# Kernel tuning notes

Measured on AMD Instinct MI355X. Metric: run time of the kernel, lower is better.

## Reference

```python
import jax, jax.numpy as jnp
import numpy as np

EPS = 1e-5


def setup_inputs() -> dict:
    key = jax.random.key(0)
    S, B, I, H, D = 256, 512, 64, 128, 32
    ks = jax.random.split(key, 12)

    def w(k, shape, fan):
        return jax.random.normal(k, shape, jnp.float32) * (fan ** -0.5)

    lengths = jax.random.randint(ks[0], (B,), 1, S + 1)
    lengths = lengths.at[0].set(S)  # ensure max length == S
    return {
        'x': jax.random.normal(ks[1], (S, B, I), jnp.float32),
        'x_d': jax.random.normal(ks[2], (S, B, D), jnp.float32),
        'lengths': lengths,
        'bn_g': jnp.ones((I,), jnp.float32), 'bn_b': jnp.zeros((I,), jnp.float32),
        'bnd_g': jnp.ones((D,), jnp.float32), 'bnd_b': jnp.zeros((D,), jnp.float32),
        'Wih': w(ks[3], (3 * H, I), I), 'Whh': w(ks[4], (3 * H, H), H),
        'bih': jnp.zeros((3 * H,), jnp.float32), 'bhh': jnp.zeros((3 * H,), jnp.float32),
        'attn_W': w(ks[5], (H, H), H), 'attn_b': jnp.zeros((H,), jnp.float32),
        'W1': w(ks[6], (H, H + D), H + D), 'b1': jnp.zeros((H,), jnp.float32),
        'W2': w(ks[7], (H, H), H), 'b2': jnp.zeros((H,), jnp.float32),
        'W3': w(ks[8], (H, H), H), 'b3': jnp.zeros((H,), jnp.float32),
    }


def reference(x, x_d, lengths, bn_g, bn_b, bnd_g, bnd_b, Wih, Whh, bih, bhh,
              attn_W, attn_b, W1, b1, W2, b2, W3, b3):
    S, B, I = x.shape
    H = Whh.shape[1]
    mask = jnp.arange(S)[:, None] < lengths[None, :]          # [S,B] valid-token mask
    mf = mask[..., None].astype(x.dtype)                       # [S,B,1]
    cnt = mf.sum()

    def bn(v, g, b):  # training-mode BatchNorm1d over the packed (valid) tokens
        mu = (v * mf).sum((0, 1)) / cnt
        var = (((v - mu) * mf) ** 2).sum((0, 1)) / cnt
        return (v - mu) * jax.lax.rsqrt(var + EPS) * g + b

    xn = bn(x, bn_g, bn_b)
    xdn = bn(x_d, bnd_g, bnd_b)

    # --- GRU (PyTorch gate order r,z,n) over padded sequence with mask ---
    h0 = jnp.zeros((B, H), x.dtype)

    def step(h, inp):
        xt, mt = inp                                           # xt [B,I], mt [B,1]
        gi = xt @ Wih.T + bih
        gh = h @ Whh.T + bhh
        ir, iz, inn = jnp.split(gi, 3, axis=-1)
        hr, hz, hn = jnp.split(gh, 3, axis=-1)
        r = jax.nn.sigmoid(ir + hr)
        z = jax.nn.sigmoid(iz + hz)
        n = jnp.tanh(inn + r * hn)
        hnew = (1 - z) * n + z * h
        hnext = jnp.where(mt, hnew, h)                         # carry last valid state
        return hnext, jnp.where(mt, hnew, 0.0)                 # padded outputs are 0

    h_last, ys = jax.lax.scan(step, h0, (xn, mf))              # ys [S,B,H]

    # --- Dynamic_Attention: per step i only position j=i survives the causal
    # mask in column k=i, so the dim-0 softmax is over one element -> weight 1.
    # Keep fc in the graph (zero grad, same as torch) via a size-1 softmax. ---
    s = (ys @ attn_W.T + attn_b).sum(-1)                       # [S,B]
    attn = jax.nn.softmax(s[..., None, None], axis=-2)[..., 0, :]  # ones [S,B,1]
    y = attn * ys

    # --- per-token MLP (dropout = identity at eval), vectorized over all tokens ---
    z0 = jnp.concatenate([y, xdn], axis=-1)                    # [S,B,H+D]
    d = jax.nn.relu(z0 @ W1.T + b1)
    d = jax.nn.relu(d @ W2.T + b2)
    d = jax.nn.relu(d @ W3.T + b3)
    out = d * mf                                               # zero padded positions
    return out, h_last[None]                                   # hidden: [1,B,H]
```

## Files before the change

### kernel.cpp

```cpp
#include <hip/hip_runtime.h>
#include <hip/hip_bf16.h>

#define SS 256
#define BB 512
#define II 64
#define HH 128
#define DD 32

typedef __attribute__((ext_vector_type(8))) short short8;
typedef __attribute__((ext_vector_type(4))) float f32x4;

__device__ __forceinline__ short f2bf(float f) {
    unsigned u = __builtin_bit_cast(unsigned, f);
    u += 0x7FFFu + ((u >> 16) & 1u);
    return (short)(u >> 16);
}
__device__ __forceinline__ int pack2bf(float a, float b) {
    return (int)((((unsigned)(unsigned short)f2bf(b)) << 16) |
                  ((unsigned)(unsigned short)f2bf(a)));
}
__device__ __forceinline__ short8 load8bf(const float* p) {
    short8 r;
#pragma unroll
    for (int j = 0; j < 8; ++j) r[j] = f2bf(p[j]);
    return r;
}

__device__ __forceinline__ void sync_lds() {
    __builtin_amdgcn_s_waitcnt(0xc07f);
    __builtin_amdgcn_s_barrier();
}

__global__ __launch_bounds__(256) void stats_kernel(
    const float* __restrict__ x, const float* __restrict__ xd,
    const int* __restrict__ lengths, double* __restrict__ acc)
{
    __shared__ float red_s[256];
    __shared__ float red_q[256];
    const int rows = SS * BB;
    int blk = blockIdx.x;
    const float* v;
    int C, rpb, base;
    if (blk < 256) { v = x;  C = II; rpb = rows / 256; base = 0; }
    else           { v = xd; C = DD; rpb = rows / 128; base = 128; blk -= 256; }

    const int tid = threadIdx.x;
    const int c   = tid & (C - 1);
    const int rg  = tid / C;
    const int rpg = 256 / C;
    const int r0  = blk * rpb;
    const int r1  = r0 + rpb;
    float s = 0.f, q = 0.f;
    for (int r = r0 + rg; r < r1; r += rpg) {
        const int b  = r & (BB - 1);
        const int si = r >> 9;
        if (si < lengths[b]) {
            const float xv = v[(size_t)r * C + c];
            s += xv;
            q  = fmaf(xv, xv, q);
        }
    }
    red_s[tid] = s; red_q[tid] = q;
    __syncthreads();
    if (rg == 0) {
        for (int g = 1; g < rpg; ++g) { s += red_s[c + g * C]; q += red_q[c + g * C]; }
        atomicAdd(&acc[base + c],     (double)s);
        atomicAdd(&acc[base + C + c], (double)q);
    }
}

__global__ __launch_bounds__(128) void finalize_kernel(
    const int* __restrict__ lengths, const double* __restrict__ acc,
    const float* __restrict__ bn_g, const float* __restrict__ bn_b,
    const float* __restrict__ bnd_g, const float* __restrict__ bnd_b,
    float* __restrict__ der)
{
    __shared__ int redc[128];
    __shared__ double s_inv;
    const int tid = threadIdx.x;
    int cs = 0;
    for (int i = tid; i < BB; i += 128) cs += lengths[i];
    redc[tid] = cs;
    __syncthreads();
    if (tid == 0) {
        int tot = 0;
        for (int i = 0; i < 128; ++i) tot += redc[i];
        s_inv = 1.0 / (double)tot;
    }
    __syncthreads();
    const double inv = s_inv;
    if (tid < 64) {
        const double mu  = acc[tid] * inv;
        const double var = acc[64 + tid] * inv - mu * mu;
        const float  rs  = rsqrtf((float)(var + 1e-5));
        const float  a   = rs * bn_g[tid];
        der[tid]      = a;
        der[64 + tid] = bn_b[tid] - (float)mu * a;
    } else if (tid < 96) {
        const int i = tid - 64;
        const double mu  = acc[128 + i] * inv;
        const double var = acc[160 + i] * inv - mu * mu;
        const float  rs  = rsqrtf((float)(var + 1e-5));
        const float  a   = rs * bnd_g[i];
        der[128 + i] = a;
        der[160 + i] = bnd_b[i] - (float)mu * a;
    }
}

__global__ __launch_bounds__(512, 2) void gru_kernel(
    const float* __restrict__ x, const int* __restrict__ lengths,
    const float* __restrict__ Wih, const float* __restrict__ Whh,
    const float* __restrict__ bih, const float* __restrict__ bhh,
    const float* __restrict__ der,
    float* __restrict__ ys, float* __restrict__ hlast)
{
    __shared__ __align__(16) short hbf[2][16 * 136];
    __shared__ __align__(16) short xbf[2][16 * 72];

    const int tid  = threadIdx.x;
    const int w    = tid >> 6;
    const int l    = tid & 63;
    const int col  = l & 15;
    const int quad = l >> 4;
    const int b0   = blockIdx.x * 16;
    const int ur   = 16 * w + col;
    const int g0   = 16 * w + quad * 4;

    short8 WR[6], WZ[6], WNh[4], WNx[2];
#pragma unroll
    for (int ks = 0; ks < 4; ++ks) {
        const int ko = ks * 32 + quad * 8;
        WR[ks]  = load8bf(&Whh[(size_t)ur * HH + ko]);
        WZ[ks]  = load8bf(&Whh[(size_t)(HH + ur) * HH + ko]);
        WNh[ks] = load8bf(&Whh[(size_t)(2 * HH + ur) * HH + ko]);
    }
#pragma unroll
    for (int ks = 0; ks < 2; ++ks) {
        const int ko = ks * 32 + quad * 8;
        WR[4 + ks] = load8bf(&Wih[(size_t)ur * II + ko]);
        WZ[4 + ks] = load8bf(&Wih[(size_t)(HH + ur) * II + ko]);
        WNx[ks]    = load8bf(&Wih[(size_t)(2 * HH + ur) * II + ko]);
    }
    float br_[4], bz_[4], bnh_[4], bnx_[4];
#pragma unroll
    for (int r = 0; r < 4; ++r) {
        const int g = g0 + r;
        br_[r]  = bih[g] + bhh[g];
        bz_[r]  = bih[HH + g] + bhh[HH + g];
        bnh_[r] = bhh[2 * HH + g];
        bnx_[r] = bih[2 * HH + g];
    }
    const int len = lengths[b0 + col];

    const int srow = tid >> 5, scol = (tid & 31) * 2;
    const float ax0 = der[scol],      ax1 = der[scol + 1];
    const float cx0 = der[64 + scol], cx1 = der[64 + scol + 1];

    for (int i = tid; i < 16 * 136 / 2; i += 512) ((int*)hbf[0])[i] = 0;
    float hreg[4] = {0.f, 0.f, 0.f, 0.f};
    {
        const float2 xv = *(const float2*)&x[(size_t)(b0 + srow) * II + scol];
        *(int*)&xbf[0][srow * 72 + scol] =
            pack2bf(fmaf(xv.x, ax0, cx0), fmaf(xv.y, ax1, cx1));
    }
    sync_lds();

    int p = 0;
    for (int t = 0; t < SS; ++t) {
        float2 xv;
        if (t + 1 < SS)
            xv = *(const float2*)&x[(size_t)((t + 1) * BB + b0 + srow) * II + scol];

        short8 Hf[4];
#pragma unroll
        for (int ks = 0; ks < 4; ++ks)
            Hf[ks] = *(const short8*)&hbf[p][col * 136 + ks * 32 + quad * 8];
        const short8 XN0 = *(const short8*)&xbf[p][col * 72 + quad * 8];
        const short8 XN1 = *(const short8*)&xbf[p][col * 72 + 32 + quad * 8];

        f32x4 ar  = {br_[0],  br_[1],  br_[2],  br_[3]};
        f32x4 az  = {bz_[0],  bz_[1],  bz_[2],  bz_[3]};
        f32x4 anh = {bnh_[0], bnh_[1], bnh_[2], bnh_[3]};
        f32x4 anx = {bnx_[0], bnx_[1], bnx_[2], bnx_[3]};
#pragma unroll
        for (int ks = 0; ks < 4; ++ks) {
            ar  = __builtin_amdgcn_mfma_f32_16x16x32_bf16(WR[ks],  Hf[ks], ar,  0, 0, 0);
            az  = __builtin_amdgcn_mfma_f32_16x16x32_bf16(WZ[ks],  Hf[ks], az,  0, 0, 0);
            anh = __builtin_amdgcn_mfma_f32_16x16x32_bf16(WNh[ks], Hf[ks], anh, 0, 0, 0);
        }
        ar  = __builtin_amdgcn_mfma_f32_16x16x32_bf16(WR[4],  XN0, ar,  0, 0, 0);
        ar  = __builtin_amdgcn_mfma_f32_16x16x32_bf16(WR[5],  XN1, ar,  0, 0, 0);
        az  = __builtin_amdgcn_mfma_f32_16x16x32_bf16(WZ[4],  XN0, az,  0, 0, 0);
        az  = __builtin_amdgcn_mfma_f32_16x16x32_bf16(WZ[5],  XN1, az,  0, 0, 0);
        anx = __builtin_amdgcn_mfma_f32_16x16x32_bf16(WNx[0], XN0, anx, 0, 0, 0);
        anx = __builtin_amdgcn_mfma_f32_16x16x32_bf16(WNx[1], XN1, anx, 0, 0, 0);

        const bool valid = (t < len);
#pragma unroll
        for (int r = 0; r < 4; ++r) {
            const float rg = __builtin_amdgcn_rcpf(1.f + __expf(-ar[r]));
            const float zg = __builtin_amdgcn_rcpf(1.f + __expf(-az[r]));
            const float nv = anx[r] + rg * anh[r];
            const float ng = 1.f - 2.f * __builtin_amdgcn_rcpf(1.f + __expf(2.f * nv));
            const float hnew = (1.f - zg) * ng + zg * hreg[r];
            hreg[r] = valid ? hnew : hreg[r];
        }
        {
            float4 o;
            o.x = hreg[0]; o.y = hreg[1]; o.z = hreg[2]; o.w = hreg[3];
            *(float4*)&ys[((size_t)t * BB + b0 + col) * HH + g0] = o;
            int2 pk;
            pk.x = pack2bf(hreg[0], hreg[1]);
            pk.y = pack2bf(hreg[2], hreg[3]);
            *(int2*)&hbf[p ^ 1][col * 136 + g0] = pk;
        }
        if (t + 1 < SS)
            *(int*)&xbf[p ^ 1][srow * 72 + scol] =
                pack2bf(fmaf(xv.x, ax0, cx0), fmaf(xv.y, ax1, cx1));

        sync_lds();
        p ^= 1;
    }

    {
        float4 hl;
        hl.x = hreg[0]; hl.y = hreg[1]; hl.z = hreg[2]; hl.w = hreg[3];
        *(float4*)&hlast[(size_t)(b0 + col) * HH + g0] = hl;
    }
}

__global__ __launch_bounds__(512, 2) void mlp_kernel(
    const float* __restrict__ xd, const int* __restrict__ lengths,
    const float* __restrict__ W1, const float* __restrict__ b1v,
    const float* __restrict__ W2, const float* __restrict__ b2v,
    const float* __restrict__ W3, const float* __restrict__ b3v,
    const float* __restrict__ der, float* io)
{
    __shared__ __align__(16) short z0[2][16 * 168];
    __shared__ __align__(16) short d1b[2][16 * 136];
    __shared__ __align__(16) short d2b[2][16 * 136];

    const int tid  = threadIdx.x;
    const int w    = tid >> 6;
    const int l    = tid & 63;
    const int col  = l & 15;
    const int quad = l >> 4;
    const int ur   = 16 * w + col;
    const int g0   = 16 * w + quad * 4;

    short8 F1[5], F2[4], F3[4];
#pragma unroll
    for (int ks = 0; ks < 5; ++ks)
        F1[ks] = load8bf(&W1[(size_t)ur * 160 + ks * 32 + quad * 8]);
#pragma unroll
    for (int ks = 0; ks < 4; ++ks) {
        const int ko = ks * 32 + quad * 8;
        F2[ks] = load8bf(&W2[(size_t)ur * HH + ko]);
        F3[ks] = load8bf(&W3[(size_t)ur * HH + ko]);
    }
    float bb1_[4], bb2_[4], bb3_[4];
#pragma unroll
    for (int r = 0; r < 4; ++r) {
        bb1_[r] = b1v[g0 + r]; bb2_[r] = b2v[g0 + r]; bb3_[r] = b3v[g0 + r];
    }

    const int yrow = tid >> 5, yc = (tid & 31) * 4;
    const int drow = tid >> 4, dcol = (tid & 15) * 2;
    float ad0 = 0.f, ad1 = 0.f, cd0 = 0.f, cd1 = 0.f;
    if (tid < 256) {
        ad0 = der[128 + dcol]; ad1 = der[128 + dcol + 1];
        cd0 = der[160 + dcol]; cd1 = der[160 + dcol + 1];
    }

    const int tile0 = blockIdx.x * 16;

    {
        const size_t tok0 = (size_t)tile0 * 16;
        const float4 yv = *(const float4*)&io[(tok0 + yrow) * HH + yc];
        int2 pk;
        pk.x = pack2bf(yv.x, yv.y);
        pk.y = pack2bf(yv.z, yv.w);
        *(int2*)&z0[0][yrow * 168 + yc] = pk;
        if (tid < 256) {
            const float2 dv = *(const float2*)&xd[(tok0 + drow) * DD + dcol];
            *(int*)&z0[0][drow * 168 + HH + dcol] =
                pack2bf(fmaf(dv.x, ad0, cd0), fmaf(dv.y, ad1, cd1));
        }
    }
    sync_lds();

    int p = 0;
    for (int it = 0; it <= 17; ++it) {
        float4 yv; float2 dv;
        const int nt = it + 1;
        if (nt <= 15) {
            const size_t tok0n = (size_t)(tile0 + nt) * 16;
            yv = *(const float4*)&io[(tok0n + yrow) * HH + yc];
            if (tid < 256) dv = *(const float2*)&xd[(tok0n + drow) * DD + dcol];
        }

        f32x4 a1 = {bb1_[0], bb1_[1], bb1_[2], bb1_[3]};
#pragma unroll
        for (int ks = 0; ks < 5; ++ks)
            a1 = __builtin_amdgcn_mfma_f32_16x16x32_bf16(
                F1[ks], *(const short8*)&z0[p][col * 168 + ks * 32 + quad * 8], a1, 0, 0, 0);
        {
            int2 pk;
            pk.x = pack2bf(fmaxf(a1[0], 0.f), fmaxf(a1[1], 0.f));
            pk.y = pack2bf(fmaxf(a1[2], 0.f), fmaxf(a1[3], 0.f));
            *(int2*)&d1b[p ^ 1][col * 136 + g0] = pk;
        }

        f32x4 a2 = {bb2_[0], bb2_[1], bb2_[2], bb2_[3]};
#pragma unroll
        for (int ks = 0; ks < 4; ++ks)
            a2 = __builtin_amdgcn_mfma_f32_16x16x32_bf16(
                F2[ks], *(const short8*)&d1b[p][col * 136 + ks * 32 + quad * 8], a2, 0, 0, 0);
        {
            int2 pk;
            pk.x = pack2bf(fmaxf(a2[0], 0.f), fmaxf(a2[1], 0.f));
            pk.y = pack2bf(fmaxf(a2[2], 0.f), fmaxf(a2[3], 0.f));
            *(int2*)&d2b[p ^ 1][col * 136 + g0] = pk;
        }

        f32x4 a3 = {bb3_[0], bb3_[1], bb3_[2], bb3_[3]};
#pragma unroll
        for (int ks = 0; ks < 4; ++ks)
            a3 = __builtin_amdgcn_mfma_f32_16x16x32_bf16(
                F3[ks], *(const short8*)&d2b[p][col * 136 + ks * 32 + quad * 8], a3, 0, 0, 0);
        if (it >= 2) {
            const int tok0 = (tile0 + it - 2) * 16;
            const int tI = tok0 >> 9;
            const int bI = tok0 & (BB - 1);
            const bool v = tI < lengths[bI + col];
            float4 o;
            o.x = v ? fmaxf(a3[0], 0.f) : 0.f;
            o.y = v ? fmaxf(a3[1], 0.f) : 0.f;
            o.z = v ? fmaxf(a3[2], 0.f) : 0.f;
            o.w = v ? fmaxf(a3[3], 0.f) : 0.f;
            *(float4*)&io[((size_t)tok0 + col) * HH + g0] = o;
        }

        if (nt <= 15) {
            int2 pk;
            pk.x = pack2bf(yv.x, yv.y);
            pk.y = pack2bf(yv.z, yv.w);
            *(int2*)&z0[p ^ 1][yrow * 168 + yc] = pk;
            if (tid < 256)
                *(int*)&z0[p ^ 1][drow * 168 + HH + dcol] =
                    pack2bf(fmaf(dv.x, ad0, cd0), fmaf(dv.y, ad1, cd1));
        }
        sync_lds();
        p ^= 1;
    }
}

extern "C" void kernel_launch(void* const* d_in, const int* in_sizes, int n_in,
                              void* d_out, int out_size, void* d_ws, size_t ws_size,
                              hipStream_t stream)
{
    (void)in_sizes; (void)n_in; (void)out_size; (void)ws_size;
    const float* x     = (const float*)d_in[0];
    const float* xd    = (const float*)d_in[1];
    const int*   lens  = (const int*)d_in[2];
    const float* bn_g  = (const float*)d_in[3];
    const float* bn_b  = (const float*)d_in[4];
    const float* bnd_g = (const float*)d_in[5];
    const float* bnd_b = (const float*)d_in[6];
    const float* Wih   = (const float*)d_in[7];
    const float* Whh   = (const float*)d_in[8];
    const float* bih   = (const float*)d_in[9];
    const float* bhh   = (const float*)d_in[10];
    const float* W1    = (const float*)d_in[13];
    const float* b1    = (const float*)d_in[14];
    const float* W2    = (const float*)d_in[15];
    const float* b2    = (const float*)d_in[16];
    const float* W3    = (const float*)d_in[17];
    const float* b3    = (const float*)d_in[18];

    float* out   = (float*)d_out;
    float* hlast = out + (size_t)SS * BB * HH;

    double* acc = (double*)d_ws;
    float*  der = (float*)((char*)d_ws + 2048);

    hipMemsetAsync(d_ws, 0, 2048, stream);

    stats_kernel<<<384, 256, 0, stream>>>(x, xd, lens, acc);
    finalize_kernel<<<1, 128, 0, stream>>>(lens, acc, bn_g, bn_b, bnd_g, bnd_b, der);

    gru_kernel<<<BB / 16, 512, 0, stream>>>(x, lens, Wih, Whh, bih, bhh, der,
                                            out, hlast);

    mlp_kernel<<<512, 512, 0, stream>>>(xd, lens, W1, b1, W2, b2, W3, b3,
                                        der, out);
}
```

Baseline: 474.6 us.

## Halve GRU block to 4 waves, each computing two 16-row hidden tiles

```diff
diff --git a/kernel.cpp b/kernel.cpp
--- a/kernel.cpp
+++ b/kernel.cpp
@@ -107,7 +107,7 @@
     }
 }
 
-__global__ __launch_bounds__(512, 2) void gru_kernel(
+__global__ __launch_bounds__(256, 1) void gru_kernel(
     const float* __restrict__ x, const int* __restrict__ lengths,
     const float* __restrict__ Wih, const float* __restrict__ Whh,
     const float* __restrict__ bih, const float* __restrict__ bhh,
@@ -123,53 +123,75 @@
     const int col  = l & 15;
     const int quad = l >> 4;
     const int b0   = blockIdx.x * 16;
-    const int ur   = 16 * w + col;
-    const int g0   = 16 * w + quad * 4;
-
-    short8 WR[6], WZ[6], WNh[4], WNx[2];
+    const int ur0  = 32 * w + col;
+    const int ur1  = ur0 + 16;
+    const int g0   = 32 * w + quad * 4;
+    const int g1   = g0 + 16;
+
+    short8 WR0[6], WZ0[6], WNh0[4], WNx0[2];
+    short8 WR1[6], WZ1[6], WNh1[4], WNx1[2];
 #pragma unroll
     for (int ks = 0; ks < 4; ++ks) {
         const int ko = ks * 32 + quad * 8;
-        WR[ks]  = load8bf(&Whh[(size_t)ur * HH + ko]);
-        WZ[ks]  = load8bf(&Whh[(size_t)(HH + ur) * HH + ko]);
-        WNh[ks] = load8bf(&Whh[(size_t)(2 * HH + ur) * HH + ko]);
+        WR0[ks]  = load8bf(&Whh[(size_t)ur0 * HH + ko]);
+        WR1[ks]  = load8bf(&Whh[(size_t)ur1 * HH + ko]);
+        WZ0[ks]  = load8bf(&Whh[(size_t)(HH + ur0) * HH + ko]);
+        WZ1[ks]  = load8bf(&Whh[(size_t)(HH + ur1) * HH + ko]);
+        WNh0[ks] = load8bf(&Whh[(size_t)(2 * HH + ur0) * HH + ko]);
+        WNh1[ks] = load8bf(&Whh[(size_t)(2 * HH + ur1) * HH + ko]);
     }
 #pragma unroll
     for (int ks = 0; ks < 2; ++ks) {
         const int ko = ks * 32 + quad * 8;
-        WR[4 + ks] = load8bf(&Wih[(size_t)ur * II + ko]);
-        WZ[4 + ks] = load8bf(&Wih[(size_t)(HH + ur) * II + ko]);
-        WNx[ks]    = load8bf(&Wih[(size_t)(2 * HH + ur) * II + ko]);
-    }
-    float br_[4], bz_[4], bnh_[4], bnx_[4];
+        WR0[4 + ks] = load8bf(&Wih[(size_t)ur0 * II + ko]);
+        WR1[4 + ks] = load8bf(&Wih[(size_t)ur1 * II + ko]);
+        WZ0[4 + ks] = load8bf(&Wih[(size_t)(HH + ur0) * II + ko]);
+        WZ1[4 + ks] = load8bf(&Wih[(size_t)(HH + ur1) * II + ko]);
+        WNx0[ks]    = load8bf(&Wih[(size_t)(2 * HH + ur0) * II + ko]);
+        WNx1[ks]    = load8bf(&Wih[(size_t)(2 * HH + ur1) * II + ko]);
+    }
+    float br0_[4], bz0_[4], bnh0_[4], bnx0_[4];
+    float br1_[4], bz1_[4], bnh1_[4], bnx1_[4];
 #pragma unroll
     for (int r = 0; r < 4; ++r) {
-        const int g = g0 + r;
-        br_[r]  = bih[g] + bhh[g];
-        bz_[r]  = bih[HH + g] + bhh[HH + g];
-        bnh_[r] = bhh[2 * HH + g];
-        bnx_[r] = bih[2 * HH + g];
+        int g = g0 + r;
+        br0_[r]  = bih[g] + bhh[g];
+        bz0_[r]  = bih[HH + g] + bhh[HH + g];
+        bnh0_[r] = bhh[2 * HH + g];
+        bnx0_[r] = bih[2 * HH + g];
+        g = g1 + r;
+        br1_[r]  = bih[g] + bhh[g];
+        bz1_[r]  = bih[HH + g] + bhh[HH + g];
+        bnh1_[r] = bhh[2 * HH + g];
+        bnx1_[r] = bih[2 * HH + g];
     }
     const int len = lengths[b0 + col];
 
-    const int srow = tid >> 5, scol = (tid & 31) * 2;
-    const float ax0 = der[scol],      ax1 = der[scol + 1];
-    const float cx0 = der[64 + scol], cx1 = der[64 + scol + 1];
-
-    for (int i = tid; i < 16 * 136 / 2; i += 512) ((int*)hbf[0])[i] = 0;
-    float hreg[4] = {0.f, 0.f, 0.f, 0.f};
+    const int srow = tid >> 4, scol = (tid & 15) * 4;
+    float axc[4], cxc[4];
+#pragma unroll
+    for (int j = 0; j < 4; ++j) {
+        axc[j] = der[scol + j];
+        cxc[j] = der[64 + scol + j];
+    }
+
+    for (int i = tid; i < 16 * 136 / 2; i += 256) ((int*)hbf[0])[i] = 0;
+    float hreg0[4] = {0.f, 0.f, 0.f, 0.f};
+    float hreg1[4] = {0.f, 0.f, 0.f, 0.f};
     {
-        const float2 xv = *(const float2*)&x[(size_t)(b0 + srow) * II + scol];
-        *(int*)&xbf[0][srow * 72 + scol] =
-            pack2bf(fmaf(xv.x, ax0, cx0), fmaf(xv.y, ax1, cx1));
+        const float4 xv = *(const float4*)&x[(size_t)(b0 + srow) * II + scol];
+        int2 pk;
+        pk.x = pack2bf(fmaf(xv.x, axc[0], cxc[0]), fmaf(xv.y, axc[1], cxc[1]));
+        pk.y = pack2bf(fmaf(xv.z, axc[2], cxc[2]), fmaf(xv.w, axc[3], cxc[3]));
+        *(int2*)&xbf[0][srow * 72 + scol] = pk;
     }
     sync_lds();
 
     int p = 0;
     for (int t = 0; t < SS; ++t) {
-        float2 xv;
+        float4 xv;
         if (t + 1 < SS)
-            xv = *(const float2*)&x[(size_t)((t + 1) * BB + b0 + srow) * II + scol];
+            xv = *(const float4*)&x[(size_t)((t + 1) * BB + b0 + srow) * II + scol];
 
         short8 Hf[4];
 #pragma unroll
@@ -178,54 +200,89 @@
         const short8 XN0 = *(const short8*)&xbf[p][col * 72 + quad * 8];
         const short8 XN1 = *(const short8*)&xbf[p][col * 72 + 32 + quad * 8];
 
-        f32x4 ar  = {br_[0],  br_[1],  br_[2],  br_[3]};
-        f32x4 az  = {bz_[0],  bz_[1],  bz_[2],  bz_[3]};
-        f32x4 anh = {bnh_[0], bnh_[1], bnh_[2], bnh_[3]};
-        f32x4 anx = {bnx_[0], bnx_[1], bnx_[2], bnx_[3]};
+        f32x4 ar0  = {br0_[0],  br0_[1],  br0_[2],  br0_[3]};
+        f32x4 ar1  = {br1_[0],  br1_[1],  br1_[2],  br1_[3]};
+        f32x4 az0  = {bz0_[0],  bz0_[1],  bz0_[2],  bz0_[3]};
+        f32x4 az1  = {bz1_[0],  bz1_[1],  bz1_[2],  bz1_[3]};
+        f32x4 anh0 = {bnh0_[0], bnh0_[1], bnh0_[2], bnh0_[3]};
+        f32x4 anh1 = {bnh1_[0], bnh1_[1], bnh1_[2], bnh1_[3]};
+        f32x4 anx0 = {bnx0_[0], bnx0_[1], bnx0_[2], bnx0_[3]};
+        f32x4 anx1 = {bnx1_[0], bnx1_[1], bnx1_[2], bnx1_[3]};
 #pragma unroll
         for (int ks = 0; ks < 4; ++ks) {
-            ar  = __builtin_amdgcn_mfma_f32_16x16x32_bf16(WR[ks],  Hf[ks], ar,  0, 0, 0);
-            az  = __builtin_amdgcn_mfma_f32_16x16x32_bf16(WZ[ks],  Hf[ks], az,  0, 0, 0);
-            anh = __builtin_amdgcn_mfma_f32_16x16x32_bf16(WNh[ks], Hf[ks], anh, 0, 0, 0);
-        }
-        ar  = __builtin_amdgcn_mfma_f32_16x16x32_bf16(WR[4],  XN0, ar,  0, 0, 0);
-        ar  = __builtin_amdgcn_mfma_f32_16x16x32_bf16(WR[5],  XN1, ar,  0, 0, 0);
-        az  = __builtin_amdgcn_mfma_f32_16x16x32_bf16(WZ[4],  XN0, az,  0, 0, 0);
-        az  = __builtin_amdgcn_mfma_f32_16x16x32_bf16(WZ[5],  XN1, az,  0, 0, 0);
-        anx = __builtin_amdgcn_mfma_f32_16x16x32_bf16(WNx[0], XN0, anx, 0, 0, 0);
-        anx = __builtin_amdgcn_mfma_f32_16x16x32_bf16(WNx[1], XN1, anx, 0, 0, 0);
+            ar0  = __builtin_amdgcn_mfma_f32_16x16x32_bf16(WR0[ks],  Hf[ks], ar0,  0, 0, 0);
+            ar1  = __builtin_amdgcn_mfma_f32_16x16x32_bf16(WR1[ks],  Hf[ks], ar1,  0, 0, 0);
+            az0  = __builtin_amdgcn_mfma_f32_16x16x32_bf16(WZ0[ks],  Hf[ks], az0,  0, 0, 0);
+            az1  = __builtin_amdgcn_mfma_f32_16x16x32_bf16(WZ1[ks],  Hf[ks], az1,  0, 0, 0);
+            anh0 = __builtin_amdgcn_mfma_f32_16x16x32_bf16(WNh0[ks], Hf[ks], anh0, 0, 0, 0);
+            anh1 = __builtin_amdgcn_mfma_f32_16x16x32_bf16(WNh1[ks], Hf[ks], anh1, 0, 0, 0);
+        }
+        ar0  = __builtin_amdgcn_mfma_f32_16x16x32_bf16(WR0[4],  XN0, ar0,  0, 0, 0);
+        ar0  = __builtin_amdgcn_mfma_f32_16x16x32_bf16(WR0[5],  XN1, ar0,  0, 0, 0);
+        ar1  = __builtin_amdgcn_mfma_f32_16x16x32_bf16(WR1[4],  XN0, ar1,  0, 0, 0);
+        ar1  = __builtin_amdgcn_mfma_f32_16x16x32_bf16(WR1[5],  XN1, ar1,  0, 0, 0);
+        az0  = __builtin_amdgcn_mfma_f32_16x16x32_bf16(WZ0[4],  XN0, az0,  0, 0, 0);
+        az0  = __builtin_amdgcn_mfma_f32_16x16x32_bf16(WZ0[5],  XN1, az0,  0, 0, 0);
+        az1  = __builtin_amdgcn_mfma_f32_16x16x32_bf16(WZ1[4],  XN0, az1,  0, 0, 0);
+        az1  = __builtin_amdgcn_mfma_f32_16x16x32_bf16(WZ1[5],  XN1, az1,  0, 0, 0);
+        anx0 = __builtin_amdgcn_mfma_f32_16x16x32_bf16(WNx0[0], XN0, anx0, 0, 0, 0);
+        anx0 = __builtin_amdgcn_mfma_f32_16x16x32_bf16(WNx0[1], XN1, anx0, 0, 0, 0);
+        anx1 = __builtin_amdgcn_mfma_f32_16x16x32_bf16(WNx1[0], XN0, anx1, 0, 0, 0);
+        anx1 = __builtin_amdgcn_mfma_f32_16x16x32_bf16(WNx1[1], XN1, anx1, 0, 0, 0);
 
         const bool valid = (t < len);
 #pragma unroll
         for (int r = 0; r < 4; ++r) {
-            const float rg = __builtin_amdgcn_rcpf(1.f + __expf(-ar[r]));
-            const float zg = __builtin_amdgcn_rcpf(1.f + __expf(-az[r]));
-            const float nv = anx[r] + rg * anh[r];
-            const float ng = 1.f - 2.f * __builtin_amdgcn_rcpf(1.f + __expf(2.f * nv));
-            const float hnew = (1.f - zg) * ng + zg * hreg[r];
-            hreg[r] = valid ? hnew : hreg[r];
+            {
+                const float rg = __builtin_amdgcn_rcpf(1.f + __expf(-ar0[r]));
+                const float zg = __builtin_amdgcn_rcpf(1.f + __expf(-az0[r]));
+                const float nv = anx0[r] + rg * anh0[r];
+                const float ng = 1.f - 2.f * __builtin_amdgcn_rcpf(1.f + __expf(2.f * nv));
+                const float hnew = (1.f - zg) * ng + zg * hreg0[r];
+                hreg0[r] = valid ? hnew : hreg0[r];
+            }
+            {
+                const float rg = __builtin_amdgcn_rcpf(1.f + __expf(-ar1[r]));
+                const float zg = __builtin_amdgcn_rcpf(1.f + __expf(-az1[r]));
+                const float nv = anx1[r] + rg * anh1[r];
+                const float ng = 1.f - 2.f * __builtin_amdgcn_rcpf(1.f + __expf(2.f * nv));
+                const float hnew = (1.f - zg) * ng + zg * hreg1[r];
+                hreg1[r] = valid ? hnew : hreg1[r];
+            }
         }
         {
-            float4 o;
-            o.x = hreg[0]; o.y = hreg[1]; o.z = hreg[2]; o.w = hreg[3];
-            *(float4*)&ys[((size_t)t * BB + b0 + col) * HH + g0] = o;
+            float4 o0, o1;
+            o0.x = hreg0[0]; o0.y = hreg0[1]; o0.z = hreg0[2]; o0.w = hreg0[3];
+            o1.x = hreg1[0]; o1.y = hreg1[1]; o1.z = hreg1[2]; o1.w = hreg1[3];
+            const size_t yb = ((size_t)t * BB + b0 + col) * HH;
+            *(float4*)&ys[yb + g0] = o0;
+            *(float4*)&ys[yb + g1] = o1;
+            int2 pk0, pk1;
+            pk0.x = pack2bf(hreg0[0], hreg0[1]);
+            pk0.y = pack2bf(hreg0[2], hreg0[3]);
+            pk1.x = pack2bf(hreg1[0], hreg1[1]);
+            pk1.y = pack2bf(hreg1[2], hreg1[3]);
+            *(int2*)&hbf[p ^ 1][col * 136 + g0] = pk0;
+            *(int2*)&hbf[p ^ 1][col * 136 + g1] = pk1;
+        }
+        if (t + 1 < SS) {
             int2 pk;
-            pk.x = pack2bf(hreg[0], hreg[1]);
-            pk.y = pack2bf(hreg[2], hreg[3]);
-            *(int2*)&hbf[p ^ 1][col * 136 + g0] = pk;
-        }
-        if (t + 1 < SS)
-            *(int*)&xbf[p ^ 1][srow * 72 + scol] =
-                pack2bf(fmaf(xv.x, ax0, cx0), fmaf(xv.y, ax1, cx1));
+            pk.x = pack2bf(fmaf(xv.x, axc[0], cxc[0]), fmaf(xv.y, axc[1], cxc[1]));
+            pk.y = pack2bf(fmaf(xv.z, axc[2], cxc[2]), fmaf(xv.w, axc[3], cxc[3]));
+            *(int2*)&xbf[p ^ 1][srow * 72 + scol] = pk;
+        }
 
         sync_lds();
         p ^= 1;
     }
 
     {
-        float4 hl;
-        hl.x = hreg[0]; hl.y = hreg[1]; hl.z = hreg[2]; hl.w = hreg[3];
-        *(float4*)&hlast[(size_t)(b0 + col) * HH + g0] = hl;
+        float4 hl0, hl1;
+        hl0.x = hreg0[0]; hl0.y = hreg0[1]; hl0.z = hreg0[2]; hl0.w = hreg0[3];
+        hl1.x = hreg1[0]; hl1.y = hreg1[1]; hl1.z = hreg1[2]; hl1.w = hreg1[3];
+        const size_t hb = (size_t)(b0 + col) * HH;
+        *(float4*)&hlast[hb + g0] = hl0;
+        *(float4*)&hlast[hb + g1] = hl1;
     }
 }
 
@@ -384,12 +441,12 @@
     double* acc = (double*)d_ws;
     float*  der = (float*)((char*)d_ws + 2048);
 
-    hipMemsetAsync(d_ws, 0, 2048, stream);
+    (void)hipMemsetAsync(d_ws, 0, 2048, stream);
 
     stats_kernel<<<384, 256, 0, stream>>>(x, xd, lens, acc);
     finalize_kernel<<<1, 128, 0, stream>>>(lens, acc, bn_g, bn_b, bnd_g, bnd_b, der);
 
-    gru_kernel<<<BB / 16, 512, 0, stream>>>(x, lens, Wih, Whh, bih, bhh, der,
+    gru_kernel<<<BB / 16, 256, 0, stream>>>(x, lens, Wih, Whh, bih, bhh, der,
                                             out, hlast);
 
     mlp_kernel<<<512, 512, 0, stream>>>(xd, lens, W1, b1, W2, b2, W3, b3,
```

Result: slower. 498.5 us (+5.0%).
